# Kernel tuning notes

Measured on AMD Instinct MI355X. Metric: run time of the kernel, lower is better.

Reference implementation:

```python
import jax, jax.numpy as jnp
import numpy as np
from jax import lax

B, T, C = 4, 2048, 2048
H, S = 32, 64
HEAD_SIZE_DIVISOR = 8.0
LN_EPS = 1e-5


def setup_inputs() -> dict:
    key = jax.random.key(0)
    ks = jax.random.split(key, 12)
    scale = 0.02
    return {
        "hidden": jax.random.normal(ks[0], (B, T, C), jnp.float32),
        "state_kv": jnp.zeros((B, H, S, S), jnp.float32),
        "time_decay": jax.random.normal(ks[1], (H, S), jnp.float32) * 0.5,
        "time_faaaa": jax.random.normal(ks[2], (H, S), jnp.float32) * 0.5,
        "time_mix_key": jax.random.uniform(ks[3], (1, 1, C), jnp.float32),
        "time_mix_value": jax.random.uniform(ks[4], (1, 1, C), jnp.float32),
        "time_mix_receptance": jax.random.uniform(ks[5], (1, 1, C), jnp.float32),
        "time_mix_gate": jax.random.uniform(ks[6], (1, 1, C), jnp.float32),
        "key_w": jax.random.normal(ks[7], (C, C), jnp.float32) * scale,
        "value_w": jax.random.normal(ks[8], (C, C), jnp.float32) * scale,
        "receptance_w": jax.random.normal(ks[9], (C, C), jnp.float32) * scale,
        "gate_w": jax.random.normal(ks[10], (C, C), jnp.float32) * scale,
        "output_w": jax.random.normal(ks[11], (C, C), jnp.float32) * scale,
        "ln_w": jnp.ones((C,), jnp.float32),
        "ln_b": jnp.zeros((C,), jnp.float32),
    }


def _rwkv5_scan(r, k, v, w, u, state0):
    # r,k,v: [B,T,H,S]; w,u: [H,S]; state0: [B,H,S,S]
    w_ = w[None, :, :, None]  # decay broadcast over value dim
    u_ = u[None, :, :, None]  # time_first (bonus) broadcast over value dim

    def step(state, rkv):
        rt, kt, vt = rkv  # each [B,H,S]
        a = kt[:, :, :, None] * vt[:, :, None, :]      # outer product [B,H,S,S]
        o = jnp.einsum("bhs,bhsd->bhd", rt, u_ * a + state)
        state = a + w_ * state
        return state, o

    rt = jnp.moveaxis(r, 1, 0)  # [T,B,H,S]
    kt = jnp.moveaxis(k, 1, 0)
    vt = jnp.moveaxis(v, 1, 0)
    state_f, out = lax.scan(step, state0, (rt, kt, vt))
    return jnp.moveaxis(out, 0, 1), state_f  # [B,T,H,S], [B,H,S,S]


def reference(hidden, state_kv, time_decay, time_faaaa, time_mix_key,
              time_mix_value, time_mix_receptance, time_mix_gate,
              key_w, value_w, receptance_w, gate_w, output_w, ln_w, ln_b):
    B_, T_, C_ = hidden.shape
    H_, S_ = time_faaaa.shape

    # time shift: prepend zero row, drop last (state=None path)
    shifted = jnp.pad(hidden, ((0, 0), (1, 0), (0, 0)))[:, :-1]

    mix = lambda m: hidden * m + shifted * (1.0 - m)
    k = mix(time_mix_key) @ key_w.T
    v = mix(time_mix_value) @ value_w.T
    r = mix(time_mix_receptance) @ receptance_w.T
    gate = jax.nn.silu(mix(time_mix_gate) @ gate_w.T)

    r = r.reshape(B_, T_, H_, S_)
    k = k.reshape(B_, T_, H_, S_)
    v = v.reshape(B_, T_, H_, S_)

    w = jnp.exp(-jnp.exp(time_decay))  # [H,S]
    out, state_f = _rwkv5_scan(r, k, v, w, time_faaaa, state_kv)

    # GroupNorm over H groups of size S, applied per (b,t) row
    x = out.reshape(B_ * T_, H_, S_) / HEAD_SIZE_DIVISOR
    mu = jnp.mean(x, axis=-1, keepdims=True)
    var = jnp.var(x, axis=-1, keepdims=True)
    xn = (x - mu) * lax.rsqrt(var + LN_EPS)
    xn = xn.reshape(B_ * T_, H_ * S_) * ln_w + ln_b

    out = xn.reshape(B_, T_, C_) * gate
    out = out @ output_w.T
    return out, state_f
```

## Files before the change

kernel.cpp:

```cpp
#include <hip/hip_runtime.h>
#include <hip/hip_bf16.h>

typedef unsigned short u16;
typedef __bf16 bf16x8 __attribute__((ext_vector_type(8)));
typedef unsigned short ushort8v __attribute__((ext_vector_type(8)));
typedef float f32x4 __attribute__((ext_vector_type(4)));
typedef float f32x8 __attribute__((ext_vector_type(8)));

#define B_ 4
#define T_ 2048
#define C_ 2048
#define H_ 32
#define S_ 64

__device__ __forceinline__ u16 f2bf(float x) {
  unsigned int u = __float_as_uint(x);
  unsigned int r = (u + 0x7fffu + ((u >> 16) & 1u)) >> 16;
  return (u16)r;
}
__device__ __forceinline__ float bf2f(u16 x) {
  return __uint_as_float(((unsigned int)x) << 16);
}
__device__ __forceinline__ void gload_lds16(const void* g, void* l) {
  __builtin_amdgcn_global_load_lds(
      (const __attribute__((address_space(1))) void*)g,
      (__attribute__((address_space(3))) void*)l, 16, 0, 0);
}

#define VM10 asm volatile("s_waitcnt vmcnt(10)" ::: "memory")
#define VM8 asm volatile("s_waitcnt vmcnt(8)" ::: "memory")
#define VM4 asm volatile("s_waitcnt vmcnt(4)" ::: "memory")
#define VM0 asm volatile("s_waitcnt vmcnt(0)" ::: "memory")
#define BARR __builtin_amdgcn_s_barrier()
#define SCB __builtin_amdgcn_sched_barrier(0)

__global__ __launch_bounds__(256) void mix_cast_kernel(
    const float* __restrict__ hidden, const float* __restrict__ mixp,
    u16* __restrict__ out) {
  int idx = blockIdx.x * 256 + threadIdx.x;
  int c4 = idx & 511;
  int bt = idx >> 9;
  int t = bt & (T_ - 1);
  float4 h = reinterpret_cast<const float4*>(hidden)[idx];
  float4 m = reinterpret_cast<const float4*>(mixp)[c4];
  float4 sh = make_float4(0.f, 0.f, 0.f, 0.f);
  if (t != 0) sh = reinterpret_cast<const float4*>(hidden)[idx - 512];
  ushort4 o;
  o.x = f2bf(h.x * m.x + sh.x * (1.f - m.x));
  o.y = f2bf(h.y * m.y + sh.y * (1.f - m.y));
  o.z = f2bf(h.z * m.z + sh.z * (1.f - m.z));
  o.w = f2bf(h.w * m.w + sh.w * (1.f - m.w));
  reinterpret_cast<ushort4*>(out)[idx] = o;
}

__global__ __launch_bounds__(256) void mix4_cast_kernel(
    const float* __restrict__ hidden,
    const float* __restrict__ mK, const float* __restrict__ mV,
    const float* __restrict__ mR, const float* __restrict__ mG,
    u16* __restrict__ oK, u16* __restrict__ oV,
    u16* __restrict__ oR, u16* __restrict__ oG) {
  int idx = blockIdx.x * 256 + threadIdx.x;
  int c4 = idx & 511;
  int bt = idx >> 9;
  int t = bt & (T_ - 1);
  float4 h = reinterpret_cast<const float4*>(hidden)[idx];
  float4 sh = make_float4(0.f, 0.f, 0.f, 0.f);
  if (t != 0) sh = reinterpret_cast<const float4*>(hidden)[idx - 512];
  float4 m;
  ushort4 o;
#define DOMIX(MP, OP)                                          \
  m = reinterpret_cast<const float4*>(MP)[c4];                 \
  o.x = f2bf(h.x * m.x + sh.x * (1.f - m.x));                  \
  o.y = f2bf(h.y * m.y + sh.y * (1.f - m.y));                  \
  o.z = f2bf(h.z * m.z + sh.z * (1.f - m.z));                  \
  o.w = f2bf(h.w * m.w + sh.w * (1.f - m.w));                  \
  reinterpret_cast<ushort4*>(OP)[idx] = o;
  DOMIX(mK, oK)
  DOMIX(mV, oV)
  DOMIX(mR, oR)
  DOMIX(mG, oG)
#undef DOMIX
}

__global__ __launch_bounds__(256) void conv_bf16_kernel(
    const float* __restrict__ in, u16* __restrict__ out, int n4) {
  int i = blockIdx.x * 256 + threadIdx.x;
  if (i >= n4) return;
  float4 v = reinterpret_cast<const float4*>(in)[i];
  ushort4 o;
  o.x = f2bf(v.x); o.y = f2bf(v.y); o.z = f2bf(v.z); o.w = f2bf(v.w);
  reinterpret_cast<ushort4*>(out)[i] = o;
}

template <typename OT>
__global__ __launch_bounds__(512, 2) void gemm_bt256(
    const u16* __restrict__ A, const u16* __restrict__ Bm,
    OT* __restrict__ C, int M, int N, int K) {
  __shared__ u16 Asl[4][8192];
  __shared__ u16 Bsl[4][8192];
  const int tid = threadIdx.x, lane = tid & 63, w = tid >> 6;
  const int wr = w >> 2, wc = w & 3;
  const int a15 = lane & 15, g4 = lane >> 4;
  const int nbn = N >> 8;
  const int nwg = gridDim.x, bid = blockIdx.x, cpx = nwg >> 3;
  const int swz = (bid & 7) * cpx + (bid >> 3);
  const int bm = swz / nbn, bn = swz % nbn;
  const int Ar0 = bm * 256, Br0 = bn * 256;

  const int rowoff = w * 32 + (lane >> 2);
  const int colswz = ((lane & 3) ^ ((lane >> 3) & 3)) * 8;
  const u16* Agl = A + (size_t)(Ar0 + rowoff) * K + colswz;
  const u16* Bgl = Bm + (size_t)(Br0 + rowoff) * K + colswz;
  const int lb = w * 1024;

  const int rdc = (((lane >> 4) ^ ((lane >> 1) & 3))) * 8;
  const int arow = wr * 128 + a15;
  const int brow = wc * 64 + a15;

  f32x4 acc[8][4];
#pragma unroll
  for (int m = 0; m < 8; m++)
#pragma unroll
    for (int n = 0; n < 4; n++) acc[m][n] = (f32x4){0.f, 0.f, 0.f, 0.f};

  auto STA = [&](int ktile, int kk, int slot) {
    const u16* g = Agl + ktile * 64 + kk * 32;
    gload_lds16(g, &Asl[slot][lb]);
    gload_lds16(g + (size_t)16 * K, &Asl[slot][lb + 512]);
  };
  auto STB = [&](int ktile, int kk, int slot) {
    const u16* g = Bgl + ktile * 64 + kk * 32;
    gload_lds16(g, &Bsl[slot][lb]);
    gload_lds16(g + (size_t)16 * K, &Bsl[slot][lb + 512]);
  };
  auto PH = [&](int P, int kk, int mh) {
    const u16* As_ = Asl[P * 2 + kk];
    const u16* Bs_ = Bsl[P * 2 + kk];
    bf16x8 af[4], bv[4];
    int ab = (arow + mh * 64) * 32 + rdc;
#pragma unroll
    for (int mf = 0; mf < 4; mf++)
      af[mf] = __builtin_bit_cast(bf16x8, *reinterpret_cast<const ushort8v*>(&As_[ab + mf * 512]));
    int bb = brow * 32 + rdc;
#pragma unroll
    for (int nf = 0; nf < 4; nf++)
      bv[nf] = __builtin_bit_cast(bf16x8, *reinterpret_cast<const ushort8v*>(&Bs_[bb + nf * 512]));
    __builtin_amdgcn_s_setprio(1);
#pragma unroll
    for (int mf = 0; mf < 4; mf++)
#pragma unroll
      for (int nf = 0; nf < 4; nf++)
        acc[mh * 4 + mf][nf] =
            __builtin_amdgcn_mfma_f32_16x16x32_bf16(af[mf], bv[nf], acc[mh * 4 + mf][nf], 0, 0, 0);
    __builtin_amdgcn_s_setprio(0);
  };

  const int NT = K >> 6;
  STA(0, 0, 0); STB(0, 0, 0);
  STA(0, 1, 1); STB(0, 1, 1);
  STA(1, 0, 2); STB(1, 0, 2);

  for (int T = 0; T + 2 < NT; ++T) {
    int P = T & 1, Q = P ^ 1;
    STA(T + 1, 1, Q * 2 + 1); STB(T + 1, 1, Q * 2 + 1);
    VM10; BARR; SCB; PH(P, 0, 0); PH(P, 0, 1); BARR;
    STA(T + 2, 0, P * 2 + 0); STB(T + 2, 0, P * 2 + 0);
    VM10; BARR; SCB; PH(P, 1, 0); PH(P, 1, 1); BARR;
  }
  {
    int T = NT - 2, P = T & 1, Q = P ^ 1;
    STA(T + 1, 1, Q * 2 + 1); STB(T + 1, 1, Q * 2 + 1);
    VM10; BARR; SCB; PH(P, 0, 0); PH(P, 0, 1); BARR;
    VM8; BARR; SCB; PH(P, 1, 0); PH(P, 1, 1); BARR;
  }
  {
    int P = (NT - 1) & 1;
    VM4; BARR; SCB; PH(P, 0, 0); PH(P, 0, 1); BARR;
    VM0; BARR; SCB; PH(P, 1, 0); PH(P, 1, 1); BARR;
  }

  if constexpr (sizeof(OT) == 2) {
    u16* ep = (w < 4) ? Asl[w] : Bsl[w - 4];
#pragma unroll
    for (int mfg = 0; mfg < 8; mfg++)
#pragma unroll
      for (int q = 0; q < 4; q++)
#pragma unroll
        for (int nf = 0; nf < 4; nf++)
          ep[(mfg * 16 + g4 * 4 + q) * 64 + nf * 16 + a15] = f2bf(acc[mfg][nf][q]);
    OT* cbase = C + (size_t)(Ar0 + wr * 128) * N + Br0 + wc * 64;
#pragma unroll
    for (int i = 0; i < 16; i++) {
      int id = lane + 64 * i;
      int row = id >> 3, k16 = id & 7;
      ushort8v v8 = *reinterpret_cast<const ushort8v*>(&ep[row * 64 + k16 * 8]);
      *reinterpret_cast<ushort8v*>(cbase + (size_t)row * N + k16 * 8) = v8;
    }
  } else {
    int crow0 = Ar0 + wr * 128 + g4 * 4;
    int ccol0 = Br0 + wc * 64 + a15;
#pragma unroll
    for (int mfg = 0; mfg < 8; mfg++) {
#pragma unroll
      for (int q = 0; q < 4; q++) {
        OT* cp = C + (size_t)(crow0 + mfg * 16 + q) * N + ccol0;
#pragma unroll
        for (int nf = 0; nf < 4; nf++) cp[nf * 16] = (OT)acc[mfg][nf][q];
      }
    }
  }
}

template <int CHL>
__global__ __launch_bounds__(64) void scan_phase1_mfma(
    const u16* __restrict__ Kb, const u16* __restrict__ Vb,
    const float* __restrict__ td, float* __restrict__ chunks) {
  constexpr int NCH = T_ / CHL;
  constexpr int LDW = CHL + 8;
  __shared__ u16 Ash[64 * LDW];
  __shared__ u16 Vsh[64 * LDW];
  int lane = threadIdx.x & 63;
  int gw = blockIdx.x;
  int c = gw & (NCH - 1), bh = gw / NCH;
  int h = bh & 31, b = bh >> 5;

  size_t base = ((size_t)b * T_ + (size_t)c * CHL) * C_ + h * 64 + lane;
  const u16* Kp = Kb + base;
  const u16* Vp = Vb + base;

  {
    float w = __expf(-__expf(td[h * 64 + lane]));
    u16* Arow = &Ash[lane * LDW];
    float p = 1.f;
#pragma unroll
    for (int i4 = CHL - 4; i4 >= 0; i4 -= 4) {
      float a3 = bf2f(Kp[(size_t)(i4 + 3) * C_]) * p; p *= w;
      float a2 = bf2f(Kp[(size_t)(i4 + 2) * C_]) * p; p *= w;
      float a1 = bf2f(Kp[(size_t)(i4 + 1) * C_]) * p; p *= w;
      float a0 = bf2f(Kp[(size_t)(i4 + 0) * C_]) * p; p *= w;
      ushort4 pk;
      pk.x = f2bf(a0); pk.y = f2bf(a1); pk.z = f2bf(a2); pk.w = f2bf(a3);
      *reinterpret_cast<ushort4*>(&Arow[i4]) = pk;
    }
  }
  {
    u16* Vrow = &Vsh[lane * LDW];
#pragma unroll
    for (int i4 = 0; i4 < CHL; i4 += 4) {
      ushort4 pk;
      pk.x = Vp[(size_t)(i4 + 0) * C_];
      pk.y = Vp[(size_t)(i4 + 1) * C_];
      pk.z = Vp[(size_t)(i4 + 2) * C_];
      pk.w = Vp[(size_t)(i4 + 3) * C_];
      *reinterpret_cast<ushort4*>(&Vrow[i4]) = pk;
    }
  }

  f32x4 acc[4][4];
#pragma unroll
  for (int m = 0; m < 4; m++)
#pragma unroll
    for (int n = 0; n < 4; n++) acc[m][n] = (f32x4){0.f, 0.f, 0.f, 0.f};

#pragma unroll
  for (int kb = 0; kb < CHL / 32; kb++) {
    int ko = kb * 32 + (lane >> 4) * 8;
    bf16x8 Af[4], Bf[4];
#pragma unroll
    for (int m = 0; m < 4; m++) {
      ushort8v t8 = *reinterpret_cast<const ushort8v*>(&Ash[(m * 16 + (lane & 15)) * LDW + ko]);
      Af[m] = __builtin_bit_cast(bf16x8, t8);
    }
#pragma unroll
    for (int n = 0; n < 4; n++) {
      ushort8v t8 = *reinterpret_cast<const ushort8v*>(&Vsh[(n * 16 + (lane & 15)) * LDW + ko]);
      Bf[n] = __builtin_bit_cast(bf16x8, t8);
    }
#pragma unroll
    for (int m = 0; m < 4; m++)
#pragma unroll
      for (int n = 0; n < 4; n++)
        acc[m][n] = __builtin_amdgcn_mfma_f32_16x16x32_bf16(Af[m], Bf[n], acc[m][n], 0, 0, 0);
  }

  float* outp = chunks + (((size_t)c * B_ + b) * H_ + h) * 4096;
  int r0 = (lane >> 4) * 4, c0 = lane & 15;
#pragma unroll
  for (int m = 0; m < 4; m++)
#pragma unroll
    for (int n = 0; n < 4; n++)
#pragma unroll
      for (int q = 0; q < 4; q++)
        outp[(size_t)(m * 16 + r0 + q) * 64 + n * 16 + c0] = acc[m][n][q];
}

template <int NCH, int CHL>
__global__ __launch_bounds__(256) void scan_phase1(
    const u16* __restrict__ Kb, const u16* __restrict__ Vb,
    const float* __restrict__ td, float* __restrict__ chunks) {
  int lane = threadIdx.x & 63;
  int gw = (blockIdx.x * 256 + threadIdx.x) >> 6;
  int c = gw & (NCH - 1), bh = gw / NCH;
  int h = bh & 31, b = bh >> 5;
  const float* tdh = td + h * 64;
  float wreg[64];
#pragma unroll
  for (int s = 0; s < 64; s++) wreg[s] = __expf(-__expf(tdh[s]));
  float st[64];
#pragma unroll
  for (int s = 0; s < 64; s++) st[s] = 0.f;
  size_t base = ((size_t)b * T_ + (size_t)c * CHL) * C_ + h * 64 + lane;
  const u16* Kp = Kb + base;
  const u16* Vp = Vb + base;
  for (int t = 0; t < CHL; t++) {
    float kcur = bf2f(Kp[(size_t)t * C_]), vcur = bf2f(Vp[(size_t)t * C_]);
#pragma unroll
    for (int s = 0; s < 64; s++) {
      float ks = __shfl(kcur, s);
      st[s] = fmaf(wreg[s], st[s], ks * vcur);
    }
  }
  float* outp = chunks + (((size_t)c * B_ + b) * H_ + h) * 4096 + lane;
#pragma unroll
  for (int s = 0; s < 64; s++) outp[s * 64] = st[s];
}

template <int NCH, int CHL>
__global__ __launch_bounds__(256) void scan_phase2(
    const float* __restrict__ st0, const float* __restrict__ td,
    float* __restrict__ chunks, float* __restrict__ state_out) {
  int idx = blockIdx.x * 256 + threadIdx.x;
  int h = (idx >> 12) & 31;
  int s = (idx >> 6) & 63;
  float wL = __expf(-(float)CHL * __expf(td[h * 64 + s]));
  float st = st0[idx];
#pragma unroll
  for (int cc = 0; cc < NCH; cc++) {
    size_t off = (size_t)cc * 524288 + idx;
    float sc = chunks[off];
    chunks[off] = st;
    st = fmaf(wL, st, sc);
  }
  state_out[idx] = st;
}

__global__ __launch_bounds__(256) void scan_phase3_mfma(
    const u16* __restrict__ Rb, const u16* __restrict__ Kb,
    const u16* __restrict__ Vb, const float* __restrict__ td,
    const float* __restrict__ tf, const float* __restrict__ chunks,
    const u16* __restrict__ Gb, const float* __restrict__ lnw,
    const float* __restrict__ lnb, u16* __restrict__ Y) {
  __shared__ __align__(16) u16 smem[4][5248];
  int lane = threadIdx.x & 63, wib = threadIdx.x >> 6;
  int gw = blockIdx.x * 4 + wib;
  int c = gw & 31, bh = gw >> 5;
  int h = bh & 31, b = bh >> 5;
  int a = lane & 15, g = lane >> 4;
  int h0 = h * 64;

  u16* Kt = smem[wib];
  u16* Vt = Kt + 1024;
  u16* StT = Vt + 1024;
  u16* AT = StT + 2560;

  f32x8 sA[2], sB[2], sC[2];
#pragma unroll
  for (int kk = 0; kk < 2; kk++) {
#pragma unroll
    for (int e = 0; e < 8; e++) {
      int s = kk * 32 + g * 8 + e;
      float ew = __expf(td[h0 + s]);
      sA[kk][e] = __expf(-(float)a * ew);
      sB[kk][e] = __expf(-((float)a - 8.f) * ew);
      sC[kk][e] = __expf(-(7.f - (float)a) * ew);
    }
  }
  f32x4 sE[4];
  f32x4 ewD;
#pragma unroll
  for (int ms = 0; ms < 4; ms++) {
    ewD[ms] = __expf(td[h0 + ms * 16 + a]);
#pragma unroll
    for (int q = 0; q < 4; q++)
      sE[ms][q] = __expf(-16.f * __expf(td[h0 + ms * 16 + g * 4 + q]));
  }

  f32x4 St[4][4];
  const float* cpc = chunks + (((size_t)c * B_ + b) * H_ + h) * 4096;
#pragma unroll
  for (int ms = 0; ms < 4; ms++)
#pragma unroll
    for (int nd = 0; nd < 4; nd++)
#pragma unroll
      for (int q = 0; q < 4; q++)
        St[ms][nd][q] = cpc[(size_t)(ms * 16 + g * 4 + q) * 64 + nd * 16 + a];

#pragma unroll
  for (int z = 0; z < 6; z++) {
    int idx = z * 64 + lane;
    int row = idx / 24, col = 16 + idx % 24;
    AT[row * 40 + col] = 0;
  }

  size_t tbase = ((size_t)b * T_ + (size_t)c * 64) * C_ + h0;

  for (int sb = 0; sb < 4; sb++) {
    size_t rb0 = tbase + (size_t)(sb * 16) * C_;

    ushort8v r8[2], k8[2];
#pragma unroll
    for (int kk = 0; kk < 2; kk++) {
      r8[kk] = *reinterpret_cast<const ushort8v*>(Rb + rb0 + (size_t)a * C_ + kk * 32 + g * 8);
      k8[kk] = *reinterpret_cast<const ushort8v*>(Kb + rb0 + (size_t)a * C_ + kk * 32 + g * 8);
    }
    {
      int srow = lane >> 3;
      int scol = (lane & 7) * 8;
      *reinterpret_cast<ushort8v*>(&Kt[srow * 64 + scol]) =
          *reinterpret_cast<const ushort8v*>(Kb + rb0 + (size_t)srow * C_ + scol);
      *reinterpret_cast<ushort8v*>(&Kt[(srow + 8) * 64 + scol]) =
          *reinterpret_cast<const ushort8v*>(Kb + rb0 + (size_t)(srow + 8) * C_ + scol);
      *reinterpret_cast<ushort8v*>(&Vt[srow * 64 + scol]) =
          *reinterpret_cast<const ushort8v*>(Vb + rb0 + (size_t)srow * C_ + scol);
      *reinterpret_cast<ushort8v*>(&Vt[(srow + 8) * 64 + scol]) =
          *reinterpret_cast<const ushort8v*>(Vb + rb0 + (size_t)(srow + 8) * C_ + scol);
    }

    f32x4 O[4];
#pragma unroll
    for (int nd = 0; nd < 4; nd++) O[nd] = (f32x4){0.f, 0.f, 0.f, 0.f};

#pragma unroll
    for (int kk = 0; kk < 2; kk++) {
#pragma unroll
      for (int msl = 0; msl < 2; msl++) {
        int ms = kk * 2 + msl;
#pragma unroll
        for (int nd = 0; nd < 4; nd++) {
          ushort4 pk;
          pk.x = f2bf(St[ms][nd][0]); pk.y = f2bf(St[ms][nd][1]);
          pk.z = f2bf(St[ms][nd][2]); pk.w = f2bf(St[ms][nd][3]);
          *reinterpret_cast<ushort4*>(&StT[(a + nd * 16) * 40 + msl * 16 + g * 4]) = pk;
        }
      }
      ushort8v rt;
#pragma unroll
      for (int e = 0; e < 8; e++) rt[e] = f2bf(bf2f(r8[kk][e]) * sA[kk][e]);
      bf16x8 rtf = __builtin_bit_cast(bf16x8, rt);
#pragma unroll
      for (int nd = 0; nd < 4; nd++) {
        ushort8v sfr = *reinterpret_cast<const ushort8v*>(&StT[(a + nd * 16) * 40 + g * 8]);
        O[nd] = __builtin_amdgcn_mfma_f32_16x16x32_bf16(
            rtf, __builtin_bit_cast(bf16x8, sfr), O[nd], 0, 0, 0);
      }
    }

    float p = 0.f;
    {
      uintptr_t ta = (uintptr_t)(tf + h0);
      asm volatile("" : "+v"(ta));
      const float* tfp = (const float*)ta;
#pragma unroll
      for (int kk = 0; kk < 2; kk++) {
        float4 t0 = *reinterpret_cast<const float4*>(tfp + kk * 32 + g * 8);
        float4 t1 = *reinterpret_cast<const float4*>(tfp + kk * 32 + g * 8 + 4);
        float tv[8] = {t0.x, t0.y, t0.z, t0.w, t1.x, t1.y, t1.z, t1.w};
#pragma unroll
        for (int e = 0; e < 8; e++)
          p = fmaf(bf2f(r8[kk][e]) * tv[e], bf2f(k8[kk][e]), p);
      }
    }
    p += __shfl_xor(p, 16);
    p += __shfl_xor(p, 32);

    f32x4 Am = (f32x4){0.f, 0.f, 0.f, 0.f};
#pragma unroll
    for (int kk = 0; kk < 2; kk++) {
      ushort8v kh, rh;
#pragma unroll
      for (int e = 0; e < 8; e++) {
        kh[e] = f2bf(bf2f(k8[kk][e]) * sC[kk][e]);
        rh[e] = f2bf(bf2f(r8[kk][e]) * sB[kk][e]);
      }
      Am = __builtin_amdgcn_mfma_f32_16x16x32_bf16(
          __builtin_bit_cast(bf16x8, kh), __builtin_bit_cast(bf16x8, rh), Am, 0, 0, 0);
    }
    {
      ushort4 aw;
#pragma unroll
      for (int q = 0; q < 4; q++) {
        int jr = g * 4 + q;
        float v = (jr < a) ? Am[q] : ((jr == a) ? p : 0.f);
        ((u16*)&aw)[q] = f2bf(v);
      }
      *reinterpret_cast<ushort4*>(&AT[a * 40 + g * 4]) = aw;
    }
    bf16x8 afrag;
    {
      ushort8v t8 = *reinterpret_cast<const ushort8v*>(&AT[a * 40 + g * 8]);
      afrag = __builtin_bit_cast(bf16x8, t8);
    }

    bf16x8 vfrag[4];
#pragma unroll
    for (int nd = 0; nd < 4; nd++) {
      ushort8v t8;
      if (g < 2) {
#pragma unroll
        for (int e = 0; e < 8; e++) t8[e] = Vt[(g * 8 + e) * 64 + a + nd * 16];
      } else {
#pragma unroll
        for (int e = 0; e < 8; e++) t8[e] = 0;
      }
      vfrag[nd] = __builtin_bit_cast(bf16x8, t8);
    }

#pragma unroll
    for (int nd = 0; nd < 4; nd++)
      O[nd] = __builtin_amdgcn_mfma_f32_16x16x32_bf16(afrag, vfrag[nd], O[nd], 0, 0, 0);

#pragma unroll
    for (int ms = 0; ms < 4; ms++)
#pragma unroll
      for (int nd = 0; nd < 4; nd++)
#pragma unroll
        for (int q = 0; q < 4; q++) St[ms][nd][q] *= sE[ms][q];

#pragma unroll
    for (int ms = 0; ms < 4; ms++) {
      ushort8v kt8;
      if (g < 2) {
#pragma unroll
        for (int e = 0; e < 8; e++) {
          int j = g * 8 + e;
          float f = bf2f(Kt[j * 64 + ms * 16 + a]) * __expf(-(15.f - (float)j) * ewD[ms]);
          kt8[e] = f2bf(f);
        }
      } else {
#pragma unroll
        for (int e = 0; e < 8; e++) kt8[e] = 0;
      }
      bf16x8 kf = __builtin_bit_cast(bf16x8, kt8);
#pragma unroll
      for (int nd = 0; nd < 4; nd++)
        St[ms][nd] = __builtin_amdgcn_mfma_f32_16x16x32_bf16(kf, vfrag[nd], St[ms][nd], 0, 0, 0);
    }

#pragma unroll
    for (int nd = 0; nd < 4; nd++)
#pragma unroll
      for (int q = 0; q < 4; q++) O[nd][q] *= 0.125f;
    {
      uintptr_t la = (uintptr_t)(lnw + h0);
      uintptr_t lba = (uintptr_t)(lnb + h0);
      asm volatile("" : "+v"(la), "+v"(lba));
      const float* lwp = (const float*)la;
      const float* lbp = (const float*)lba;
#pragma unroll
      for (int q = 0; q < 4; q++) {
        float ssum = O[0][q] + O[1][q] + O[2][q] + O[3][q];
        ssum += __shfl_xor(ssum, 1); ssum += __shfl_xor(ssum, 2);
        ssum += __shfl_xor(ssum, 4); ssum += __shfl_xor(ssum, 8);
        float mean = ssum * (1.f / 64.f);
        float vv = 0.f;
#pragma unroll
        for (int nd = 0; nd < 4; nd++) {
          float d = O[nd][q] - mean;
          vv = fmaf(d, d, vv);
        }
        vv += __shfl_xor(vv, 1); vv += __shfl_xor(vv, 2);
        vv += __shfl_xor(vv, 4); vv += __shfl_xor(vv, 8);
        float rs = rsqrtf(vv * (1.f / 64.f) + 1e-5f);
        size_t rowoff = rb0 + (size_t)(g * 4 + q) * C_;
#pragma unroll
        for (int nd = 0; nd < 4; nd++) {
          float xn = (O[nd][q] - mean) * rs;
          float gv = bf2f(Gb[rowoff + nd * 16 + a]);
          float sg = gv / (1.f + __expf(-gv));
          Y[rowoff + nd * 16 + a] = f2bf((xn * lwp[nd * 16 + a] + lbp[nd * 16 + a]) * sg);
        }
      }
    }
  }
}

template <int NCH, int CHL>
__global__ __launch_bounds__(256) void scan_phase3(
    const u16* __restrict__ Rb, const u16* __restrict__ Kb,
    const u16* __restrict__ Vb, const float* __restrict__ td,
    const float* __restrict__ tf, const float* __restrict__ chunks,
    const u16* __restrict__ Gb, const float* __restrict__ lnw,
    const float* __restrict__ lnb, u16* __restrict__ Y) {
  int lane = threadIdx.x & 63;
  int gw = (blockIdx.x * 256 + threadIdx.x) >> 6;
  int c = gw & (NCH - 1), bh = gw / NCH;
  int h = bh & 31, b = bh >> 5;
  const float* tdh = td + h * 64;
  float wreg[64];
#pragma unroll
  for (int s = 0; s < 64; s++) wreg[s] = __expf(-__expf(tdh[s]));
  float u_own = tf[h * 64 + lane];
  float lw = lnw[h * 64 + lane];
  float lb = lnb[h * 64 + lane];
  float st[64];
  const float* cp = chunks + (((size_t)c * B_ + b) * H_ + h) * 4096 + lane;
#pragma unroll
  for (int s = 0; s < 64; s++) st[s] = cp[s * 64];
  size_t base = ((size_t)b * T_ + (size_t)c * CHL) * C_ + h * 64 + lane;
  const u16* Rp = Rb + base;
  const u16* Kp = Kb + base;
  const u16* Vp = Vb + base;
  const u16* Gp = Gb + base;
  u16* Yp = Y + base;
  for (int t = 0; t < CHL; t++) {
    float rcur = bf2f(Rp[(size_t)t * C_]);
    float kcur = bf2f(Kp[(size_t)t * C_]);
    float vcur = bf2f(Vp[(size_t)t * C_]);
    float p = rcur * u_own * kcur;
#pragma unroll
    for (int off = 32; off >= 1; off >>= 1) p += __shfl_xor(p, off);
    float acc = 0.f;
#pragma unroll
    for (int s = 0; s < 64; s++) {
      float rs = __shfl(rcur, s);
      float ks = __shfl(kcur, s);
      acc = fmaf(rs, st[s], acc);
      st[s] = fmaf(wreg[s], st[s], ks * vcur);
    }
    float o = fmaf(p, vcur, acc);
    float x = o * 0.125f;
    float sum = x;
#pragma unroll
    for (int off = 32; off >= 1; off >>= 1) sum += __shfl_xor(sum, off);
    float mean = sum * (1.f / 64.f);
    float d = x - mean;
    float v2 = d * d;
#pragma unroll
    for (int off = 32; off >= 1; off >>= 1) v2 += __shfl_xor(v2, off);
    float var = v2 * (1.f / 64.f);
    float xn = d * rsqrtf(var + 1e-5f);
    float gg = bf2f(Gp[(size_t)t * C_]);
    float sg = gg / (1.f + __expf(-gg));
    Yp[(size_t)t * C_] = f2bf((xn * lw + lb) * sg);
  }
}

extern "C" void kernel_launch(void* const* d_in, const int* in_sizes, int n_in,
                              void* d_out, int out_size, void* d_ws, size_t ws_size,
                              hipStream_t stream) {
  const float* hidden = (const float*)d_in[0];
  const float* state0 = (const float*)d_in[1];
  const float* td = (const float*)d_in[2];
  const float* tf = (const float*)d_in[3];
  const float* mk = (const float*)d_in[4];
  const float* mv = (const float*)d_in[5];
  const float* mr = (const float*)d_in[6];
  const float* mg = (const float*)d_in[7];
  const float* kw = (const float*)d_in[8];
  const float* vw = (const float*)d_in[9];
  const float* rw = (const float*)d_in[10];
  const float* gw = (const float*)d_in[11];
  const float* ow = (const float*)d_in[12];
  const float* lnw = (const float*)d_in[13];
  const float* lnb = (const float*)d_in[14];

  float* out = (float*)d_out;
  float* state_f = out + (size_t)B_ * T_ * C_;

  const size_t MBe = (size_t)B_ * T_ * C_;
  const size_t chunks32 = (size_t)32 * B_ * H_ * S_ * S_ * 4;

  size_t bigNeed = 4 * MBe * 2 + (size_t)C_ * C_ * 2 + 4 * MBe * 2 + chunks32;
  bool useBig = (ws_size >= bigNeed);

  dim3 blk(256);
  int mixGrid = (B_ * T_ * C_ / 4) / 256;
  int convN4 = C_ * C_ / 4;
  int convGrid = convN4 / 256;
  int gemmGrid = (B_ * T_ / 256) * (C_ / 256);
  dim3 gblk(512);

  if (useBig) {
    char* ws = (char*)d_ws;
    u16* mixR = (u16*)ws;  ws += MBe * 2;
    u16* mixK = (u16*)ws;  ws += MBe * 2;
    u16* mixV = (u16*)ws;  ws += MBe * 2;
    u16* mixG = (u16*)ws;  ws += MBe * 2;
    u16* wb = (u16*)ws;    ws += (size_t)C_ * C_ * 2;
    u16* rb = (u16*)ws;    ws += MBe * 2;
    u16* kb = (u16*)ws;    ws += MBe * 2;
    u16* vb = (u16*)ws;    ws += MBe * 2;
    u16* gb = (u16*)ws;    ws += MBe * 2;
    float* chunks = (float*)ws;

    mix4_cast_kernel<<<mixGrid, blk, 0, stream>>>(hidden, mk, mv, mr, mg,
                                                  mixK, mixV, mixR, mixG);
    conv_bf16_kernel<<<convGrid, blk, 0, stream>>>(rw, wb, convN4);
    gemm_bt256<u16><<<gemmGrid, gblk, 0, stream>>>(mixR, wb, rb, B_ * T_, C_, C_);
    conv_bf16_kernel<<<convGrid, blk, 0, stream>>>(kw, wb, convN4);
    gemm_bt256<u16><<<gemmGrid, gblk, 0, stream>>>(mixK, wb, kb, B_ * T_, C_, C_);
    conv_bf16_kernel<<<convGrid, blk, 0, stream>>>(vw, wb, convN4);
    gemm_bt256<u16><<<gemmGrid, gblk, 0, stream>>>(mixV, wb, vb, B_ * T_, C_, C_);
    conv_bf16_kernel<<<convGrid, blk, 0, stream>>>(gw, wb, convN4);
    gemm_bt256<u16><<<gemmGrid, gblk, 0, stream>>>(mixG, wb, gb, B_ * T_, C_, C_);

    scan_phase1_mfma<64><<<B_ * H_ * 32, dim3(64), 0, stream>>>(kb, vb, td, chunks);
    scan_phase2<32, 64><<<2048, blk, 0, stream>>>(state0, td, chunks, state_f);
    scan_phase3_mfma<<<(B_ * H_ * 32) / 4, blk, 0, stream>>>(rb, kb, vb, td, tf, chunks, gb, lnw, lnb, mixR);

    conv_bf16_kernel<<<convGrid, blk, 0, stream>>>(ow, wb, convN4);
    gemm_bt256<float><<<gemmGrid, gblk, 0, stream>>>(mixR, wb, out, B_ * T_, C_, C_);
    return;
  }

  char* ws = (char*)d_ws;
  u16* mixA = (u16*)ws;    ws += MBe * 2;
  u16* wb = (u16*)ws;      ws += (size_t)C_ * C_ * 2;
  u16* rb = (u16*)ws;      ws += MBe * 2;
  u16* kb = (u16*)ws;      ws += MBe * 2;
  u16* vb = (u16*)ws;      ws += MBe * 2;
  u16* gb = (u16*)ws;      ws += MBe * 2;
  float* chunks = (float*)ws;
  size_t fixed = (size_t)(ws - (char*)d_ws);
  bool use32 = (ws_size >= fixed + chunks32);

  mix_cast_kernel<<<mixGrid, blk, 0, stream>>>(hidden, mr, mixA);
  conv_bf16_kernel<<<convGrid, blk, 0, stream>>>(rw, wb, convN4);
  gemm_bt256<u16><<<gemmGrid, gblk, 0, stream>>>(mixA, wb, rb, B_ * T_, C_, C_);
  mix_cast_kernel<<<mixGrid, blk, 0, stream>>>(hidden, mk, mixA);
  conv_bf16_kernel<<<convGrid, blk, 0, stream>>>(kw, wb, convN4);
  gemm_bt256<u16><<<gemmGrid, gblk, 0, stream>>>(mixA, wb, kb, B_ * T_, C_, C_);
  mix_cast_kernel<<<mixGrid, blk, 0, stream>>>(hidden, mv, mixA);
  conv_bf16_kernel<<<convGrid, blk, 0, stream>>>(vw, wb, convN4);
  gemm_bt256<u16><<<gemmGrid, gblk, 0, stream>>>(mixA, wb, vb, B_ * T_, C_, C_);
  mix_cast_kernel<<<mixGrid, blk, 0, stream>>>(hidden, mg, mixA);
  conv_bf16_kernel<<<convGrid, blk, 0, stream>>>(gw, wb, convN4);
  gemm_bt256<u16><<<gemmGrid, gblk, 0, stream>>>(mixA, wb, gb, B_ * T_, C_, C_);

  if (use32) {
    scan_phase1_mfma<64><<<B_ * H_ * 32, dim3(64), 0, stream>>>(kb, vb, td, chunks);
    scan_phase2<32, 64><<<2048, blk, 0, stream>>>(state0, td, chunks, state_f);
    scan_phase3_mfma<<<(B_ * H_ * 32) / 4, blk, 0, stream>>>(rb, kb, vb, td, tf, chunks, gb, lnw, lnb, mixA);
  } else {
    scan_phase1<16, 128><<<(B_ * H_ * 16) / 4, blk, 0, stream>>>(kb, vb, td, chunks);
    scan_phase2<16, 128><<<2048, blk, 0, stream>>>(state0, td, chunks, state_f);
    scan_phase3<16, 128><<<(B_ * H_ * 16) / 4, blk, 0, stream>>>(rb, kb, vb, td, tf, chunks, gb, lnw, lnb, mixA);
  }

  conv_bf16_kernel<<<convGrid, blk, 0, stream>>>(ow, wb, convN4);
  gemm_bt256<float><<<gemmGrid, gblk, 0, stream>>>(mixA, wb, out, B_ * T_, C_, C_);
}
```

Measured before the change: 709.9 us.

## Batch four weight casts into one launch and merge GEMM inner phases

```diff
diff --git a/kernel.cpp b/kernel.cpp
--- a/kernel.cpp
+++ b/kernel.cpp
@@ -92,6 +92,21 @@
   reinterpret_cast<ushort4*>(out)[i] = o;
 }
 
+__global__ __launch_bounds__(256) void conv4_bf16_kernel(
+    const float* __restrict__ w0, const float* __restrict__ w1,
+    const float* __restrict__ w2, const float* __restrict__ w3,
+    u16* __restrict__ o0, u16* __restrict__ o1,
+    u16* __restrict__ o2, u16* __restrict__ o3) {
+  int wsel = blockIdx.x >> 12;
+  int i = (blockIdx.x & 4095) * 256 + threadIdx.x;
+  const float* in = (wsel == 0) ? w0 : (wsel == 1) ? w1 : (wsel == 2) ? w2 : w3;
+  u16* out = (wsel == 0) ? o0 : (wsel == 1) ? o1 : (wsel == 2) ? o2 : o3;
+  float4 v = reinterpret_cast<const float4*>(in)[i];
+  ushort4 o;
+  o.x = f2bf(v.x); o.y = f2bf(v.y); o.z = f2bf(v.z); o.w = f2bf(v.w);
+  reinterpret_cast<ushort4*>(out)[i] = o;
+}
+
 template <typename OT>
 __global__ __launch_bounds__(512, 2) void gemm_bt256(
     const u16* __restrict__ A, const u16* __restrict__ Bm,
@@ -133,25 +148,25 @@
     gload_lds16(g, &Bsl[slot][lb]);
     gload_lds16(g + (size_t)16 * K, &Bsl[slot][lb + 512]);
   };
-  auto PH = [&](int P, int kk, int mh) {
+  auto PHK = [&](int P, int kk) {
     const u16* As_ = Asl[P * 2 + kk];
     const u16* Bs_ = Bsl[P * 2 + kk];
-    bf16x8 af[4], bv[4];
-    int ab = (arow + mh * 64) * 32 + rdc;
-#pragma unroll
-    for (int mf = 0; mf < 4; mf++)
-      af[mf] = __builtin_bit_cast(bf16x8, *reinterpret_cast<const ushort8v*>(&As_[ab + mf * 512]));
-    int bb = brow * 32 + rdc;
+    bf16x8 af[8], bv[4];
+#pragma unroll
+    for (int mf = 0; mf < 8; mf++)
+      af[mf] = __builtin_bit_cast(
+          bf16x8, *reinterpret_cast<const ushort8v*>(&As_[(arow + mf * 16) * 32 + rdc]));
 #pragma unroll
     for (int nf = 0; nf < 4; nf++)
-      bv[nf] = __builtin_bit_cast(bf16x8, *reinterpret_cast<const ushort8v*>(&Bs_[bb + nf * 512]));
+      bv[nf] = __builtin_bit_cast(
+          bf16x8, *reinterpret_cast<const ushort8v*>(&Bs_[(brow + nf * 16) * 32 + rdc]));
     __builtin_amdgcn_s_setprio(1);
 #pragma unroll
-    for (int mf = 0; mf < 4; mf++)
+    for (int mf = 0; mf < 8; mf++)
 #pragma unroll
       for (int nf = 0; nf < 4; nf++)
-        acc[mh * 4 + mf][nf] =
-            __builtin_amdgcn_mfma_f32_16x16x32_bf16(af[mf], bv[nf], acc[mh * 4 + mf][nf], 0, 0, 0);
+        acc[mf][nf] =
+            __builtin_amdgcn_mfma_f32_16x16x32_bf16(af[mf], bv[nf], acc[mf][nf], 0, 0, 0);
     __builtin_amdgcn_s_setprio(0);
   };
 
@@ -163,20 +178,20 @@
   for (int T = 0; T + 2 < NT; ++T) {
     int P = T & 1, Q = P ^ 1;
     STA(T + 1, 1, Q * 2 + 1); STB(T + 1, 1, Q * 2 + 1);
-    VM10; BARR; SCB; PH(P, 0, 0); PH(P, 0, 1); BARR;
+    VM10; BARR; SCB; PHK(P, 0); BARR;
     STA(T + 2, 0, P * 2 + 0); STB(T + 2, 0, P * 2 + 0);
-    VM10; BARR; SCB; PH(P, 1, 0); PH(P, 1, 1); BARR;
+    VM10; BARR; SCB; PHK(P, 1); BARR;
   }
   {
     int T = NT - 2, P = T & 1, Q = P ^ 1;
     STA(T + 1, 1, Q * 2 + 1); STB(T + 1, 1, Q * 2 + 1);
-    VM10; BARR; SCB; PH(P, 0, 0); PH(P, 0, 1); BARR;
-    VM8; BARR; SCB; PH(P, 1, 0); PH(P, 1, 1); BARR;
+    VM10; BARR; SCB; PHK(P, 0); BARR;
+    VM8; BARR; SCB; PHK(P, 1); BARR;
   }
   {
     int P = (NT - 1) & 1;
-    VM4; BARR; SCB; PH(P, 0, 0); PH(P, 0, 1); BARR;
-    VM0; BARR; SCB; PH(P, 1, 0); PH(P, 1, 1); BARR;
+    VM4; BARR; SCB; PHK(P, 0); BARR;
+    VM0; BARR; SCB; PHK(P, 1); BARR;
   }
 
   if constexpr (sizeof(OT) == 2) {
@@ -692,17 +707,18 @@
     u16* vb = (u16*)ws;    ws += MBe * 2;
     u16* gb = (u16*)ws;    ws += MBe * 2;
     float* chunks = (float*)ws;
+    u16* wbK = (u16*)chunks;
+    u16* wbV = wbK + (size_t)C_ * C_;
+    u16* wbG = wbV + (size_t)C_ * C_;
 
     mix4_cast_kernel<<<mixGrid, blk, 0, stream>>>(hidden, mk, mv, mr, mg,
                                                   mixK, mixV, mixR, mixG);
-    conv_bf16_kernel<<<convGrid, blk, 0, stream>>>(rw, wb, convN4);
+    conv4_bf16_kernel<<<4 * convGrid, blk, 0, stream>>>(rw, kw, vw, gw,
+                                                        wb, wbK, wbV, wbG);
     gemm_bt256<u16><<<gemmGrid, gblk, 0, stream>>>(mixR, wb, rb, B_ * T_, C_, C_);
-    conv_bf16_kernel<<<convGrid, blk, 0, stream>>>(kw, wb, convN4);
-    gemm_bt256<u16><<<gemmGrid, gblk, 0, stream>>>(mixK, wb, kb, B_ * T_, C_, C_);
-    conv_bf16_kernel<<<convGrid, blk, 0, stream>>>(vw, wb, convN4);
-    gemm_bt256<u16><<<gemmGrid, gblk, 0, stream>>>(mixV, wb, vb, B_ * T_, C_, C_);
-    conv_bf16_kernel<<<convGrid, blk, 0, stream>>>(gw, wb, convN4);
-    gemm_bt256<u16><<<gemmGrid, gblk, 0, stream>>>(mixG, wb, gb, B_ * T_, C_, C_);
+    gemm_bt256<u16><<<gemmGrid, gblk, 0, stream>>>(mixK, wbK, kb, B_ * T_, C_, C_);
+    gemm_bt256<u16><<<gemmGrid, gblk, 0, stream>>>(mixV, wbV, vb, B_ * T_, C_, C_);
+    gemm_bt256<u16><<<gemmGrid, gblk, 0, stream>>>(mixG, wbG, gb, B_ * T_, C_, C_);
 
     scan_phase1_mfma<64><<<B_ * H_ * 32, dim3(64), 0, stream>>>(kb, vb, td, chunks);
     scan_phase2<32, 64><<<2048, blk, 0, stream>>>(state0, td, chunks, state_f);
```

Result: no change. 696.6 us (-1.9%).
